# Kernel optimization log

Hardware: AMD Instinct MI355X
Metric: run time of the kernel (lower is better)

Reference implementation:

```python
import jax, jax.numpy as jnp
import numpy as np

B, N = 16, 128
DN0, DE0, DH = 64, 16, 128  # input node dim, input edge dim, hidden dim


def _gnn2(A, x, e, w_msg, b_msg, w_node, b_node):
    """One GNN2 layer on dense batched graphs.
    A: [B,N,N] adjacency mask, x: [B,N,Dn], e: [B,N,N,De].
    Message/new-edge: relu(Linear([x_i, x_j, e_ij])) masked by A.
    New node: relu(Linear([x, sum_j msg_ij])).
    The concat-Linear is decomposed into three matmuls to avoid
    materializing the [B,N,N,2Dn+De] concat tensor.
    """
    Dn = x.shape[-1]
    Wi, Wj, We = w_msg[:Dn], w_msg[Dn:2 * Dn], w_msg[2 * Dn:]
    xi = x @ Wi                                   # [B,N,Do]
    xj = x @ Wj                                   # [B,N,Do]
    msg = jax.nn.relu(xi[:, :, None, :] + xj[:, None, :, :] + e @ We + b_msg)
    msg = msg * A[..., None]                      # mask non-edges -> new edge_attr [B,N,N,Do]
    agg = msg.sum(axis=2)                         # scatter-sum over neighbors j -> [B,N,Do]
    Wx, Wa = w_node[:Dn], w_node[Dn:]
    x_new = jax.nn.relu(x @ Wx + agg @ Wa + b_node)
    return x_new, msg


def setup_inputs() -> dict:
    key = jax.random.key(0)
    ks = iter(jax.random.split(key, 32))
    s = 0.05
    inp = {
        "edge_index": jax.random.randint(next(ks), (B, N, N), 0, 2, dtype=jnp.int32),
        "x": jax.random.normal(next(ks), (B, N, DN0), dtype=jnp.float32),
        "edge_attr": jax.random.normal(next(ks), (B, N, N, DE0), dtype=jnp.float32),
    }
    def w(shape):
        return s * jax.random.normal(next(ks), shape, dtype=jnp.float32)
    # layer 0: node_in=64, edge_in=16 -> 128
    inp["w_msg_0"], inp["b_msg_0"] = w((2 * DN0 + DE0, DH)), w((DH,))
    inp["w_node_0"], inp["b_node_0"] = w((DN0 + DH, DH)), w((DH,))
    # layers 1,2: 128 -> 128
    for l in (1, 2):
        inp[f"w_msg_{l}"], inp[f"b_msg_{l}"] = w((2 * DH + DH, DH)), w((DH,))
        inp[f"w_node_{l}"], inp[f"b_node_{l}"] = w((DH + DH, DH)), w((DH,))
    # head mlp: 128 -> 128 -> 128 -> 1
    inp["w_h1"], inp["b_h1"] = w((DH, DH)), w((DH,))
    inp["w_h2"], inp["b_h2"] = w((DH, DH)), w((DH,))
    inp["w_h3"], inp["b_h3"] = w((DH, 1)), w((1,))
    return inp


def reference(edge_index, x, edge_attr,
              w_msg_0, b_msg_0, w_node_0, b_node_0,
              w_msg_1, b_msg_1, w_node_1, b_node_1,
              w_msg_2, b_msg_2, w_node_2, b_node_2,
              w_h1, b_h1, w_h2, b_h2, w_h3, b_h3):
    A = edge_index.astype(jnp.float32)
    x = x.astype(jnp.float32)
    # layer 0
    x, e = _gnn2(A, x, edge_attr, w_msg_0, b_msg_0, w_node_0, b_node_0)
    # middle layer with 0.5 residual blend
    x_, e_ = _gnn2(A, x, e, w_msg_1, b_msg_1, w_node_1, b_node_1)
    x = 0.5 * (x + x_)
    e = 0.5 * (e + e_)
    # last layer
    x, e = _gnn2(A, x, e, w_msg_2, b_msg_2, w_node_2, b_node_2)
    # edge_mean readout + MLP head
    h = e.mean(axis=(1, 2))                       # [B, DH]
    h = jax.nn.relu(h @ w_h1 + b_h1)
    h = jax.nn.relu(h @ w_h2 + b_h2)
    out = h @ w_h3 + b_h3                         # [B, 1]
    return out.squeeze(-1)                        # [B]
```

## Files before the change

kernel.cpp:

```cpp
#include <hip/hip_runtime.h>

constexpr int B = 16, N = 128, D = 128, DN0 = 64, DE0 = 16;

typedef _Float16 half8 __attribute__((ext_vector_type(8)));
typedef _Float16 half4 __attribute__((ext_vector_type(4)));
typedef float floatx4 __attribute__((ext_vector_type(4)));
typedef float floatx16 __attribute__((ext_vector_type(16)));

__device__ __forceinline__ void gld16(const _Float16* g, _Float16* l) {
  __builtin_amdgcn_global_load_lds(
      (const __attribute__((address_space(1))) void*)g,
      (__attribute__((address_space(3))) void*)l, 16, 0, 0);
}

__global__ __launch_bounds__(256) void k_pre(
    const float* __restrict__ x, const float* __restrict__ wm0,
    const float* __restrict__ bm0, const float* __restrict__ wm1,
    const float* __restrict__ wm2,
    float* __restrict__ xi0, float* __restrict__ xj0,
    _Float16* __restrict__ weT1, _Float16* __restrict__ weT2) {
  const int bid = blockIdx.x;
  const int t = threadIdx.x;
  if (bid < 512) {
    const int r0 = bid * 4;
    const int half = t >> 7, c = t & 127;
    __shared__ float sX[4][DN0];
    ((float*)sX)[t] = x[(size_t)r0 * DN0 + t];
    __syncthreads();
    float acc[4];
    #pragma unroll
    for (int r = 0; r < 4; ++r) acc[r] = half ? 0.f : bm0[c];
    const float* wb0 = wm0 + half * DN0 * D;
    #pragma unroll 4
    for (int k4 = 0; k4 < DN0; k4 += 4) {
      const float* wb = wb0 + k4 * D + c;
      const float w0 = wb[0], w1 = wb[D], w2 = wb[2 * D], w3 = wb[3 * D];
      #pragma unroll
      for (int r = 0; r < 4; ++r) {
        const float4 xv = *(const float4*)&sX[r][k4];
        acc[r] = fmaf(xv.x, w0, acc[r]);
        acc[r] = fmaf(xv.y, w1, acc[r]);
        acc[r] = fmaf(xv.z, w2, acc[r]);
        acc[r] = fmaf(xv.w, w3, acc[r]);
      }
    }
    float* dst = half ? xj0 : xi0;
    #pragma unroll
    for (int r = 0; r < 4; ++r) dst[(size_t)(r0 + r) * D + c] = acc[r];
  } else {
    const int g = (bid - 512) * 256 + t;
    const int layer = g >> 14;
    const int rem = g & 16383;
    const int c = rem >> 7, k = rem & 127;
    const float* src = layer ? wm2 : wm1;
    _Float16* dst = layer ? weT2 : weT1;
    dst[rem] = (_Float16)src[(2 * D + k) * D + c];
  }
}

__global__ __launch_bounds__(256) void k_edge0(
    const int* __restrict__ ei, const float* __restrict__ eattr,
    const float* __restrict__ wm0,
    const float* __restrict__ xi0, const float* __restrict__ xj0,
    _Float16* __restrict__ msg0, float* __restrict__ agg0) {
  const int row = blockIdx.x;
  const int b = row >> 7;
  const int t = threadIdx.x;
  const int c8 = (t & 15) * 8, jr = t >> 4;

  __shared__ float eb[N * 20];
  __shared__ float w_t[DE0][D];
  __shared__ float amask[N];
  __shared__ float xi_r[D];
  float* hp = eb;

  const float4* esrc = (const float4*)(eattr + (size_t)row * N * DE0);
  const float4* wsrc = (const float4*)(wm0 + 2 * DN0 * D);
  #pragma unroll
  for (int u = 0; u < 2; ++u) {
    const int idx4 = u * 256 + t;
    const int j = idx4 >> 2;
    const int k4 = (idx4 & 3) * 4;
    *(float4*)&eb[j * 20 + k4] = esrc[idx4];
    ((float4*)&w_t[0][0])[idx4] = wsrc[idx4];
  }
  if (t < N) {
    amask[t] = (float)ei[(size_t)row * N + t];
    xi_r[t] = xi0[(size_t)row * D + t];
  }
  __syncthreads();

  float acc[8][8] = {};
  #pragma unroll 4
  for (int k = 0; k < DE0; ++k) {
    float av[8];
    #pragma unroll
    for (int p = 0; p < 8; ++p) av[p] = eb[(16 * p + jr) * 20 + k];
    const floatx4 wv0 = *(const floatx4*)&w_t[k][c8];
    const floatx4 wv1 = *(const floatx4*)&w_t[k][c8 + 4];
    #pragma unroll
    for (int p = 0; p < 8; ++p)
      #pragma unroll
      for (int q = 0; q < 4; ++q) {
        acc[p][q]     = fmaf(av[p], wv0[q], acc[p][q]);
        acc[p][4 + q] = fmaf(av[p], wv1[q], acc[p][4 + q]);
      }
  }

  float acc8[8] = {};
  const float* xjb = xj0 + (size_t)b * N * D;
  _Float16* mrow = msg0 + (size_t)row * N * D;
  const floatx4 xiv0 = *(const floatx4*)&xi_r[c8];
  const floatx4 xiv1 = *(const floatx4*)&xi_r[c8 + 4];
  #pragma unroll
  for (int p = 0; p < 8; ++p) {
    const int j = 16 * p + jr;
    const float am = amask[j];
    const floatx4 xjv0 = *(const floatx4*)&xjb[j * D + c8];
    const floatx4 xjv1 = *(const floatx4*)&xjb[j * D + c8 + 4];
    half8 hv;
    #pragma unroll
    for (int q = 0; q < 4; ++q) {
      float v0 = fmaxf(xiv0[q] + xjv0[q] + acc[p][q], 0.f) * am;
      float v1 = fmaxf(xiv1[q] + xjv1[q] + acc[p][4 + q], 0.f) * am;
      hv[q] = (_Float16)v0;
      hv[4 + q] = (_Float16)v1;
      acc8[q] += v0;
      acc8[4 + q] += v1;
    }
    *(half8*)&mrow[j * D + (((t & 15) ^ jr) << 3)] = hv;
  }

  __syncthreads();
  #pragma unroll
  for (int q = 0; q < 8; ++q) hp[(jr * 16 + (t & 15)) * 8 + q] = acc8[q];
  __syncthreads();
  if (t < D) {
    float s = 0.f;
    #pragma unroll
    for (int g = 0; g < 16; ++g) s += hp[(g * 16 + (t >> 3)) * 8 + (t & 7)];
    agg0[(size_t)row * D + t] = s;
  }
}

__global__ __launch_bounds__(256) void k_node1(
    const float* __restrict__ x0, const float* __restrict__ agg0,
    const float* __restrict__ wn0, const float* __restrict__ bn0,
    const float* __restrict__ wm1, const float* __restrict__ bm1,
    float* __restrict__ x1, float* __restrict__ xi1, float* __restrict__ xj1) {
  const int r0 = blockIdx.x * 4;
  const int t = threadIdx.x;
  const int c = t & 127, rh = t >> 7;
  __shared__ float sIn[4][DN0];
  __shared__ float sAg[4][D];
  __shared__ float sX1[4][D];
  ((float*)sIn)[t] = x0[(size_t)r0 * DN0 + t];
  ((float2*)sAg)[t] = ((const float2*)(agg0 + (size_t)r0 * D))[t];
  __syncthreads();

  float acc[2];
  #pragma unroll
  for (int r = 0; r < 2; ++r) acc[r] = bn0[c];
  #pragma unroll 4
  for (int k4 = 0; k4 < DN0; k4 += 4) {
    const float* wb = wn0 + k4 * D + c;
    const float w0 = wb[0], w1 = wb[D], w2 = wb[2 * D], w3 = wb[3 * D];
    #pragma unroll
    for (int r = 0; r < 2; ++r) {
      const float4 xv = *(const float4*)&sIn[rh * 2 + r][k4];
      acc[r] = fmaf(xv.x, w0, acc[r]);
      acc[r] = fmaf(xv.y, w1, acc[r]);
      acc[r] = fmaf(xv.z, w2, acc[r]);
      acc[r] = fmaf(xv.w, w3, acc[r]);
    }
  }
  #pragma unroll 4
  for (int k4 = 0; k4 < D; k4 += 4) {
    const float* wb = wn0 + (DN0 + k4) * D + c;
    const float w0 = wb[0], w1 = wb[D], w2 = wb[2 * D], w3 = wb[3 * D];
    #pragma unroll
    for (int r = 0; r < 2; ++r) {
      const float4 xv = *(const float4*)&sAg[rh * 2 + r][k4];
      acc[r] = fmaf(xv.x, w0, acc[r]);
      acc[r] = fmaf(xv.y, w1, acc[r]);
      acc[r] = fmaf(xv.z, w2, acc[r]);
      acc[r] = fmaf(xv.w, w3, acc[r]);
    }
  }
  #pragma unroll
  for (int r = 0; r < 2; ++r) {
    const float v = fmaxf(acc[r], 0.f);
    sX1[rh * 2 + r][c] = v;
    x1[(size_t)(r0 + rh * 2 + r) * D + c] = v;
  }
  __syncthreads();

  float a[4];
  #pragma unroll
  for (int r = 0; r < 4; ++r) a[r] = rh ? 0.f : bm1[c];
  const float* wh = wm1 + (size_t)rh * D * D;
  #pragma unroll 4
  for (int k4 = 0; k4 < D; k4 += 4) {
    const float* wb = wh + k4 * D + c;
    const float w0 = wb[0], w1 = wb[D], w2 = wb[2 * D], w3 = wb[3 * D];
    #pragma unroll
    for (int r = 0; r < 4; ++r) {
      const float4 xv = *(const float4*)&sX1[r][k4];
      a[r] = fmaf(xv.x, w0, a[r]);
      a[r] = fmaf(xv.y, w1, a[r]);
      a[r] = fmaf(xv.z, w2, a[r]);
      a[r] = fmaf(xv.w, w3, a[r]);
    }
  }
  float* dst = rh ? xj1 : xi1;
  #pragma unroll
  for (int r = 0; r < 4; ++r) dst[(size_t)(r0 + r) * D + c] = a[r];
}

__global__ __launch_bounds__(256, 2) void k_mid(
    const int* __restrict__ ei, const _Float16* __restrict__ weT1,
    const _Float16* __restrict__ weT2,
    const float* __restrict__ xi, const float* __restrict__ xj,
    _Float16* __restrict__ em,
    float* __restrict__ agg1) {
  const int row = blockIdx.x;
  const int b = row >> 7;
  const int t = threadIdx.x;
  const int w = t >> 6;
  const int lane = t & 63;
  const int l31 = lane & 31;
  const int l15 = lane & 15;
  const int hl = lane >> 5;

  __shared__ _Float16 sE[N * D];
  __shared__ float sMask[N];

  const _Float16* gsrc = em + (size_t)row * N * D;
  #pragma unroll
  for (int u = 0; u < 8; ++u) {
    const int seg = (u * 4 + w) * 512;
    gld16(gsrc + seg + lane * 8, &sE[seg]);
  }

  half8 a1[8];
  #pragma unroll
  for (int ks = 0; ks < 8; ++ks)
    a1[ks] = *(const half8*)(weT1 + (32 * w + l31) * D + 16 * ks + 8 * hl);

  floatx4 xiv[4];
  #pragma unroll
  for (int g = 0; g < 4; ++g)
    xiv[g] = *(const floatx4*)&xi[(size_t)row * D + 32 * w + 8 * g + 4 * hl];
  if (t < N) sMask[t] = (float)ei[(size_t)row * N + t];

  __syncthreads();

  float am[4];
  #pragma unroll
  for (int jt = 0; jt < 4; ++jt) am[jt] = sMask[32 * jt + l31];

  const floatx16 vzero = {0.f,0.f,0.f,0.f,0.f,0.f,0.f,0.f,
                          0.f,0.f,0.f,0.f,0.f,0.f,0.f,0.f};
  floatx16 acc[4];
  #pragma unroll
  for (int jt = 0; jt < 4; ++jt) acc[jt] = vzero;
  #pragma unroll
  for (int ks = 0; ks < 8; ++ks)
    #pragma unroll
    for (int jt = 0; jt < 4; ++jt) {
      const half8 bv = *(const half8*)
          &sE[(32 * jt + l31) * D + (((2 * ks + hl) ^ l15) << 3)];
      acc[jt] = __builtin_amdgcn_mfma_f32_32x32x16_f16(a1[ks], bv, acc[jt], 0, 0, 0);
    }

  __syncthreads();

  const float* xjb = xj + (size_t)b * N * D;
  floatx4 hacc[4];
  #pragma unroll
  for (int g = 0; g < 4; ++g) hacc[g] = (floatx4){0.f, 0.f, 0.f, 0.f};
  #pragma unroll
  for (int jt = 0; jt < 4; ++jt) {
    const int j = 32 * jt + l31;
    #pragma unroll
    for (int g = 0; g < 4; ++g) {
      const int cofs = 32 * w + 8 * g + 4 * hl;
      const int hidx = j * D + (((4 * w + g) ^ l15) << 3) + 4 * hl;
      const floatx4 xjv = *(const floatx4*)&xjb[j * D + cofs];
      const half4 m0 = *(const half4*)&sE[hidx];
      half4 mid;
      floatx4 m1;
      #pragma unroll
      for (int r = 0; r < 4; ++r) {
        const float v = xiv[g][r] + xjv[r] + acc[jt][4 * g + r];
        m1[r] = fmaxf(v, 0.f) * am[jt];
        mid[r] = (_Float16)(0.5f * ((float)m0[r] + m1[r]));
      }
      *(half4*)&sE[hidx] = mid;
      hacc[g] += m1;
    }
  }

  #pragma unroll
  for (int m = 1; m < 32; m <<= 1)
    #pragma unroll
    for (int g = 0; g < 4; ++g)
      #pragma unroll
      for (int r = 0; r < 4; ++r)
        hacc[g][r] += __shfl_xor(hacc[g][r], m, 64);
  if (l31 == 0) {
    #pragma unroll
    for (int g = 0; g < 4; ++g)
      *(floatx4*)&agg1[(size_t)row * D + 32 * w + 8 * g + 4 * hl] = hacc[g];
  }

  half8 a2[8];
  #pragma unroll
  for (int ks = 0; ks < 8; ++ks)
    a2[ks] = *(const half8*)(weT2 + (32 * w + l31) * D + 16 * ks + 8 * hl);

  __syncthreads();

  #pragma unroll
  for (int jt = 0; jt < 4; ++jt) acc[jt] = vzero;
  #pragma unroll
  for (int ks = 0; ks < 8; ++ks)
    #pragma unroll
    for (int jt = 0; jt < 4; ++jt) {
      const half8 bv = *(const half8*)
          &sE[(32 * jt + l31) * D + (((2 * ks + hl) ^ l15) << 3)];
      acc[jt] = __builtin_amdgcn_mfma_f32_32x32x16_f16(a2[ks], bv, acc[jt], 0, 0, 0);
    }

  __syncthreads();

  #pragma unroll
  for (int jt = 0; jt < 4; ++jt) {
    const int j = 32 * jt + l31;
    #pragma unroll
    for (int g = 0; g < 4; ++g) {
      const int hidx = j * D + (((4 * w + g) ^ l15) << 3) + 4 * hl;
      half4 tv;
      #pragma unroll
      for (int r = 0; r < 4; ++r) tv[r] = (_Float16)acc[jt][4 * g + r];
      *(half4*)&sE[hidx] = tv;
    }
  }

  __syncthreads();

  uint4* gdst = (uint4*)(em + (size_t)row * N * D);
  const uint4* ls = (const uint4*)sE;
  #pragma unroll
  for (int u = 0; u < 8; ++u) {
    const int idx4 = u * 256 + t;
    const int j = u * 16 + (t >> 4);
    if (sMask[j] != 0.f) gdst[idx4] = ls[idx4];
  }
}

__global__ __launch_bounds__(256) void k_node2(
    const float* __restrict__ x1, const float* __restrict__ agg1,
    const float* __restrict__ wn1, const float* __restrict__ bn1,
    const float* __restrict__ wm2, const float* __restrict__ bm2,
    float* __restrict__ xi2, float* __restrict__ xj2) {
  const int r0 = blockIdx.x * 4;
  const int t = threadIdx.x;
  const int c = t & 127, rh = t >> 7;
  __shared__ float sIn[4][D];
  __shared__ float sAg[4][D];
  __shared__ float sXm[4][D];
  ((float2*)sIn)[t] = ((const float2*)(x1 + (size_t)r0 * D))[t];
  ((float2*)sAg)[t] = ((const float2*)(agg1 + (size_t)r0 * D))[t];
  __syncthreads();

  float acc[2];
  #pragma unroll
  for (int r = 0; r < 2; ++r) acc[r] = bn1[c];
  #pragma unroll 4
  for (int k4 = 0; k4 < D; k4 += 4) {
    const float* wb = wn1 + k4 * D + c;
    const float w0 = wb[0], w1 = wb[D], w2 = wb[2 * D], w3 = wb[3 * D];
    #pragma unroll
    for (int r = 0; r < 2; ++r) {
      const float4 xv = *(const float4*)&sIn[rh * 2 + r][k4];
      acc[r] = fmaf(xv.x, w0, acc[r]);
      acc[r] = fmaf(xv.y, w1, acc[r]);
      acc[r] = fmaf(xv.z, w2, acc[r]);
      acc[r] = fmaf(xv.w, w3, acc[r]);
    }
  }
  #pragma unroll 4
  for (int k4 = 0; k4 < D; k4 += 4) {
    const float* wb = wn1 + (D + k4) * D + c;
    const float w0 = wb[0], w1 = wb[D], w2 = wb[2 * D], w3 = wb[3 * D];
    #pragma unroll
    for (int r = 0; r < 2; ++r) {
      const float4 xv = *(const float4*)&sAg[rh * 2 + r][k4];
      acc[r] = fmaf(xv.x, w0, acc[r]);
      acc[r] = fmaf(xv.y, w1, acc[r]);
      acc[r] = fmaf(xv.z, w2, acc[r]);
      acc[r] = fmaf(xv.w, w3, acc[r]);
    }
  }
  #pragma unroll
  for (int r = 0; r < 2; ++r) {
    const float v = 0.5f * (sIn[rh * 2 + r][c] + fmaxf(acc[r], 0.f));
    sXm[rh * 2 + r][c] = v;
  }
  __syncthreads();

  float a[4];
  #pragma unroll
  for (int r = 0; r < 4; ++r) a[r] = rh ? 0.f : bm2[c];
  const float* wh = wm2 + (size_t)rh * D * D;
  #pragma unroll 4
  for (int k4 = 0; k4 < D; k4 += 4) {
    const float* wb = wh + k4 * D + c;
    const float w0 = wb[0], w1 = wb[D], w2 = wb[2 * D], w3 = wb[3 * D];
    #pragma unroll
    for (int r = 0; r < 4; ++r) {
      const float4 xv = *(const float4*)&sXm[r][k4];
      a[r] = fmaf(xv.x, w0, a[r]);
      a[r] = fmaf(xv.y, w1, a[r]);
      a[r] = fmaf(xv.z, w2, a[r]);
      a[r] = fmaf(xv.w, w3, a[r]);
    }
  }
  float* dst = rh ? xj2 : xi2;
  #pragma unroll
  for (int r = 0; r < 4; ++r) dst[(size_t)(r0 + r) * D + c] = a[r];
}

__global__ __launch_bounds__(256) void k_fin(
    const int* __restrict__ ei, const _Float16* __restrict__ t2,
    const float* __restrict__ xi, const float* __restrict__ xj,
    float* __restrict__ rowsum) {
  const int row = blockIdx.x;
  const int b = row >> 7;
  const int t = threadIdx.x;
  const int c8 = (t & 15) * 8, jr = t >> 4;

  __shared__ float sMask[N];
  __shared__ float hp[16][16][8];
  if (t < N) sMask[t] = (float)ei[(size_t)row * N + t];
  float xiv[8];
  *(floatx4*)&xiv[0] = *(const floatx4*)&xi[row * D + c8];
  *(floatx4*)&xiv[4] = *(const floatx4*)&xi[row * D + c8 + 4];
  __syncthreads();

  const _Float16* src = t2 + (size_t)row * N * D;
  const float* xjb = xj + (size_t)b * N * D;
  float acc8[8] = {};
  #pragma unroll
  for (int u = 0; u < 8; ++u) {
    const int j = u * 16 + jr;
    if (sMask[j] != 0.f) {
      const half8 tv = *(const half8*)(src + j * D + (((t & 15) ^ jr) << 3));
      const floatx4 xj0 = *(const floatx4*)&xjb[j * D + c8];
      const floatx4 xj1 = *(const floatx4*)&xjb[j * D + c8 + 4];
      #pragma unroll
      for (int r = 0; r < 4; ++r) {
        acc8[r]     += fmaxf(xiv[r] + xj0[r] + (float)tv[r], 0.f);
        acc8[4 + r] += fmaxf(xiv[4 + r] + xj1[r] + (float)tv[4 + r], 0.f);
      }
    }
  }
  #pragma unroll
  for (int k = 0; k < 8; ++k) hp[jr][t & 15][k] = acc8[k];
  __syncthreads();
  if (t < D) {
    float s = 0.f;
    #pragma unroll
    for (int g = 0; g < 16; ++g) s += hp[g][t >> 3][t & 7];
    rowsum[row * D + t] = s;
  }
}

__global__ __launch_bounds__(128) void k_head(
    const float* __restrict__ rowsum,
    const float* __restrict__ w1, const float* __restrict__ b1,
    const float* __restrict__ w2, const float* __restrict__ b2,
    const float* __restrict__ w3, const float* __restrict__ b3,
    float* __restrict__ out) {
  const int b = blockIdx.x;
  const int c = threadIdx.x;
  __shared__ float hr[D], h1r[D], h2r[D];
  const float* rs = rowsum + (size_t)b * N * D;
  float s = 0.f;
  for (int i = 0; i < N; ++i) s += rs[i * D + c];
  hr[c] = s * (1.f / (N * N));
  __syncthreads();
  float a = b1[c];
  #pragma unroll 8
  for (int k = 0; k < D; ++k) a = fmaf(hr[k], w1[k * D + c], a);
  h1r[c] = fmaxf(a, 0.f);
  __syncthreads();
  a = b2[c];
  #pragma unroll 8
  for (int k = 0; k < D; ++k) a = fmaf(h1r[k], w2[k * D + c], a);
  h2r[c] = fmaxf(a, 0.f);
  __syncthreads();
  hr[c] = h2r[c] * w3[c];
  __syncthreads();
  if (c == 0) {
    float s2 = b3[0];
    for (int k = 0; k < D; ++k) s2 += hr[k];
    out[b] = s2;
  }
}

extern "C" void kernel_launch(void* const* d_in, const int* in_sizes, int n_in,
                              void* d_out, int out_size, void* d_ws, size_t ws_size,
                              hipStream_t stream) {
  const int*   ei  = (const int*)d_in[0];
  const float* x0  = (const float*)d_in[1];
  const float* ea  = (const float*)d_in[2];
  const float* wm0 = (const float*)d_in[3];
  const float* bm0 = (const float*)d_in[4];
  const float* wn0 = (const float*)d_in[5];
  const float* bn0 = (const float*)d_in[6];
  const float* wm1 = (const float*)d_in[7];
  const float* bm1 = (const float*)d_in[8];
  const float* wn1 = (const float*)d_in[9];
  const float* bn1 = (const float*)d_in[10];
  const float* wm2 = (const float*)d_in[11];
  const float* bm2 = (const float*)d_in[12];
  const float* wh1 = (const float*)d_in[15];
  const float* bh1 = (const float*)d_in[16];
  const float* wh2 = (const float*)d_in[17];
  const float* bh2 = (const float*)d_in[18];
  const float* wh3 = (const float*)d_in[19];
  const float* bh3 = (const float*)d_in[20];
  float* out = (float*)d_out;

  _Float16* msg0h = (_Float16*)d_ws;
  _Float16* weT1  = msg0h + (size_t)B * N * N * D;
  _Float16* weT2  = weT1 + D * D;
  float* f = (float*)(weT2 + D * D);
  size_t off = 0;
  const size_t R = (size_t)B * N * D;
  float* xi0  = f + off; off += R;
  float* xj0  = f + off; off += R;
  float* x1   = f + off; off += R;
  float* xi1  = f + off; off += R;
  float* xj1  = f + off; off += R;
  float* xi2  = f + off; off += R;
  float* xj2  = f + off; off += R;
  float* rsum = f + off; off += R;

  float* aggS = rsum;

  const int rows = B * N;
  k_pre  <<<512 + 128, 256, 0, stream>>>(x0, wm0, bm0, wm1, wm2,
                                         xi0, xj0, weT1, weT2);
  k_edge0<<<rows, 256, 0, stream>>>(ei, ea, wm0, xi0, xj0, msg0h, aggS);
  k_node1<<<rows / 4, 256, 0, stream>>>(x0, aggS, wn0, bn0, wm1, bm1,
                                        x1, xi1, xj1);
  k_mid  <<<rows, 256, 0, stream>>>(ei, weT1, weT2, xi1, xj1, msg0h, aggS);
  k_node2<<<rows / 4, 256, 0, stream>>>(x1, aggS, wn1, bn1, wm2, bm2,
                                        xi2, xj2);
  k_fin  <<<rows, 256, 0, stream>>>(ei, msg0h, xi2, xj2, rsum);
  k_head <<<B,    128, 0, stream>>>(rsum, wh1, bh1, wh2, bh2, wh3, bh3, out);
}
```

Measured before the change: 214.0 us.

## Give each wave its own 32 edge rows in k_mid to drop block barriers

k_mid now splits the work so each wave owns 32 neighbor rows j and computes all 128 output columns for them, rather than owning 32 output columns across all rows. Each wave touches only its own slice of shared memory, so almost every __syncthreads between the two MFMA stages is removed. The edge tile is loaded per wave with an explicit vmcnt wait, and the mask comes from a register plus shuffles instead of shared memory. The cost is that weight fragments are re-read from global or L2 inside the MFMA loop instead of staying in registers, and per-wave partial aggregates must be combined through shared memory at the end.

```diff
diff --git a/kernel.cpp b/kernel.cpp
--- a/kernel.cpp
+++ b/kernel.cpp
@@ -231,132 +231,121 @@
   const int l31 = lane & 31;
   const int l15 = lane & 15;
   const int hl = lane >> 5;
+  const int j = 32 * w + l31;
 
   __shared__ _Float16 sE[N * D];
-  __shared__ float sMask[N];
+  __shared__ float sAggP[4][D];
 
   const _Float16* gsrc = em + (size_t)row * N * D;
   #pragma unroll
   for (int u = 0; u < 8; ++u) {
-    const int seg = (u * 4 + w) * 512;
+    const int seg = w * 4096 + u * 512;
     gld16(gsrc + seg + lane * 8, &sE[seg]);
   }
 
-  half8 a1[8];
+  const float am = (float)ei[(size_t)row * N + j];
+
+  asm volatile("s_waitcnt vmcnt(0)" ::: "memory");
+  __builtin_amdgcn_sched_barrier(0);
+
+  half8 bv[8];
   #pragma unroll
   for (int ks = 0; ks < 8; ++ks)
-    a1[ks] = *(const half8*)(weT1 + (32 * w + l31) * D + 16 * ks + 8 * hl);
-
-  floatx4 xiv[4];
-  #pragma unroll
-  for (int g = 0; g < 4; ++g)
-    xiv[g] = *(const floatx4*)&xi[(size_t)row * D + 32 * w + 8 * g + 4 * hl];
-  if (t < N) sMask[t] = (float)ei[(size_t)row * N + t];
-
-  __syncthreads();
-
-  float am[4];
-  #pragma unroll
-  for (int jt = 0; jt < 4; ++jt) am[jt] = sMask[32 * jt + l31];
+    bv[ks] = *(const half8*)&sE[j * D + (((2 * ks + hl) ^ l15) << 3)];
 
   const floatx16 vzero = {0.f,0.f,0.f,0.f,0.f,0.f,0.f,0.f,
                           0.f,0.f,0.f,0.f,0.f,0.f,0.f,0.f};
   floatx16 acc[4];
   #pragma unroll
-  for (int jt = 0; jt < 4; ++jt) acc[jt] = vzero;
-  #pragma unroll
-  for (int ks = 0; ks < 8; ++ks)
-    #pragma unroll
-    for (int jt = 0; jt < 4; ++jt) {
-      const half8 bv = *(const half8*)
-          &sE[(32 * jt + l31) * D + (((2 * ks + hl) ^ l15) << 3)];
-      acc[jt] = __builtin_amdgcn_mfma_f32_32x32x16_f16(a1[ks], bv, acc[jt], 0, 0, 0);
-    }
-
-  __syncthreads();
+  for (int ct = 0; ct < 4; ++ct) acc[ct] = vzero;
+  #pragma unroll
+  for (int ct = 0; ct < 4; ++ct)
+    #pragma unroll
+    for (int ks = 0; ks < 8; ++ks) {
+      const half8 av = *(const half8*)
+          &weT1[(32 * ct + l31) * D + 16 * ks + 8 * hl];
+      acc[ct] = __builtin_amdgcn_mfma_f32_32x32x16_f16(av, bv[ks], acc[ct], 0, 0, 0);
+    }
 
   const float* xjb = xj + (size_t)b * N * D;
-  floatx4 hacc[4];
-  #pragma unroll
-  for (int g = 0; g < 4; ++g) hacc[g] = (floatx4){0.f, 0.f, 0.f, 0.f};
-  #pragma unroll
-  for (int jt = 0; jt < 4; ++jt) {
-    const int j = 32 * jt + l31;
+  const float* xir = xi + (size_t)row * D;
+  #pragma unroll
+  for (int ct = 0; ct < 4; ++ct) {
+    floatx4 hacc[4];
+    #pragma unroll
+    for (int g = 0; g < 4; ++g) hacc[g] = (floatx4){0.f, 0.f, 0.f, 0.f};
     #pragma unroll
     for (int g = 0; g < 4; ++g) {
-      const int cofs = 32 * w + 8 * g + 4 * hl;
-      const int hidx = j * D + (((4 * w + g) ^ l15) << 3) + 4 * hl;
-      const floatx4 xjv = *(const floatx4*)&xjb[j * D + cofs];
+      const int co = 32 * ct + 8 * g + 4 * hl;
+      const int hidx = j * D + (((4 * ct + g) ^ l15) << 3) + 4 * hl;
+      const floatx4 xiv = *(const floatx4*)&xir[co];
+      const floatx4 xjv = *(const floatx4*)&xjb[j * D + co];
       const half4 m0 = *(const half4*)&sE[hidx];
       half4 mid;
       floatx4 m1;
       #pragma unroll
       for (int r = 0; r < 4; ++r) {
-        const float v = xiv[g][r] + xjv[r] + acc[jt][4 * g + r];
-        m1[r] = fmaxf(v, 0.f) * am[jt];
+        const float v = xiv[r] + xjv[r] + acc[ct][4 * g + r];
+        m1[r] = fmaxf(v, 0.f) * am;
         mid[r] = (_Float16)(0.5f * ((float)m0[r] + m1[r]));
       }
       *(half4*)&sE[hidx] = mid;
       hacc[g] += m1;
     }
-  }
-
-  #pragma unroll
-  for (int m = 1; m < 32; m <<= 1)
-    #pragma unroll
-    for (int g = 0; g < 4; ++g)
-      #pragma unroll
-      for (int r = 0; r < 4; ++r)
-        hacc[g][r] += __shfl_xor(hacc[g][r], m, 64);
-  if (l31 == 0) {
-    #pragma unroll
-    for (int g = 0; g < 4; ++g)
-      *(floatx4*)&agg1[(size_t)row * D + 32 * w + 8 * g + 4 * hl] = hacc[g];
-  }
-
-  half8 a2[8];
+    #pragma unroll
+    for (int m = 1; m < 32; m <<= 1)
+      #pragma unroll
+      for (int g = 0; g < 4; ++g)
+        #pragma unroll
+        for (int r = 0; r < 4; ++r)
+          hacc[g][r] += __shfl_xor(hacc[g][r], m, 64);
+    if (l31 == 0) {
+      #pragma unroll
+      for (int g = 0; g < 4; ++g)
+        *(floatx4*)&sAggP[w][32 * ct + 8 * g + 4 * hl] = hacc[g];
+    }
+  }
+
+  half8 bv2[8];
   #pragma unroll
   for (int ks = 0; ks < 8; ++ks)
-    a2[ks] = *(const half8*)(weT2 + (32 * w + l31) * D + 16 * ks + 8 * hl);
-
-  __syncthreads();
-
-  #pragma unroll
-  for (int jt = 0; jt < 4; ++jt) acc[jt] = vzero;
-  #pragma unroll
-  for (int ks = 0; ks < 8; ++ks)
-    #pragma unroll
-    for (int jt = 0; jt < 4; ++jt) {
-      const half8 bv = *(const half8*)
-          &sE[(32 * jt + l31) * D + (((2 * ks + hl) ^ l15) << 3)];
-      acc[jt] = __builtin_amdgcn_mfma_f32_32x32x16_f16(a2[ks], bv, acc[jt], 0, 0, 0);
-    }
-
-  __syncthreads();
-
-  #pragma unroll
-  for (int jt = 0; jt < 4; ++jt) {
-    const int j = 32 * jt + l31;
+    bv2[ks] = *(const half8*)&sE[j * D + (((2 * ks + hl) ^ l15) << 3)];
+  #pragma unroll
+  for (int ct = 0; ct < 4; ++ct) acc[ct] = vzero;
+  #pragma unroll
+  for (int ct = 0; ct < 4; ++ct)
+    #pragma unroll
+    for (int ks = 0; ks < 8; ++ks) {
+      const half8 av = *(const half8*)
+          &weT2[(32 * ct + l31) * D + 16 * ks + 8 * hl];
+      acc[ct] = __builtin_amdgcn_mfma_f32_32x32x16_f16(av, bv2[ks], acc[ct], 0, 0, 0);
+    }
+
+  #pragma unroll
+  for (int ct = 0; ct < 4; ++ct)
     #pragma unroll
     for (int g = 0; g < 4; ++g) {
-      const int hidx = j * D + (((4 * w + g) ^ l15) << 3) + 4 * hl;
+      const int hidx = j * D + (((4 * ct + g) ^ l15) << 3) + 4 * hl;
       half4 tv;
       #pragma unroll
-      for (int r = 0; r < 4; ++r) tv[r] = (_Float16)acc[jt][4 * g + r];
+      for (int r = 0; r < 4; ++r) tv[r] = (_Float16)acc[ct][4 * g + r];
       *(half4*)&sE[hidx] = tv;
     }
-  }
-
-  __syncthreads();
 
   uint4* gdst = (uint4*)(em + (size_t)row * N * D);
   const uint4* ls = (const uint4*)sE;
   #pragma unroll
   for (int u = 0; u < 8; ++u) {
-    const int idx4 = u * 256 + t;
-    const int j = u * 16 + (t >> 4);
-    if (sMask[j] != 0.f) gdst[idx4] = ls[idx4];
-  }
+    const int cc = u * 64 + lane;
+    const int idx4 = w * 512 + cc;
+    const float mv = __shfl(am, cc >> 4, 64);
+    if (mv != 0.f) gdst[idx4] = ls[idx4];
+  }
+
+  __syncthreads();
+  if (t < D)
+    agg1[(size_t)row * D + t] =
+        sAggP[0][t] + sAggP[1][t] + sAggP[2][t] + sAggP[3][t];
 }
 
 __global__ __launch_bounds__(256) void k_node2(
```

After: 257.0 us. 1.2x slower.

## Recompute layer-0 edge messages inside k_mid instead of storing them

Applied to the files above, without the earlier changes.

k_edge0 now only computes the aggregated sums and no longer writes the fp16 layer-0 message tensor. k_mid recomputes the layer-0 messages directly into shared memory from edge_attr, the edge weight slice and xi0/xj0. This removes a full B*N*N*D fp16 write and the matching read, which is a large memory round trip. The cost is doing the small K=16 edge matmul twice, plus extra shared memory and register pressure in k_mid, which may reduce its occupancy.

```diff
diff --git a/kernel.cpp b/kernel.cpp
--- a/kernel.cpp
+++ b/kernel.cpp
@@ -6,12 +6,6 @@
 typedef _Float16 half4 __attribute__((ext_vector_type(4)));
 typedef float floatx4 __attribute__((ext_vector_type(4)));
 typedef float floatx16 __attribute__((ext_vector_type(16)));
-
-__device__ __forceinline__ void gld16(const _Float16* g, _Float16* l) {
-  __builtin_amdgcn_global_load_lds(
-      (const __attribute__((address_space(1))) void*)g,
-      (__attribute__((address_space(3))) void*)l, 16, 0, 0);
-}
 
 __global__ __launch_bounds__(256) void k_pre(
     const float* __restrict__ x, const float* __restrict__ wm0,
@@ -62,7 +56,7 @@
     const int* __restrict__ ei, const float* __restrict__ eattr,
     const float* __restrict__ wm0,
     const float* __restrict__ xi0, const float* __restrict__ xj0,
-    _Float16* __restrict__ msg0, float* __restrict__ agg0) {
+    float* __restrict__ agg0) {
   const int row = blockIdx.x;
   const int b = row >> 7;
   const int t = threadIdx.x;
@@ -109,7 +103,6 @@
 
   float acc8[8] = {};
   const float* xjb = xj0 + (size_t)b * N * D;
-  _Float16* mrow = msg0 + (size_t)row * N * D;
   const floatx4 xiv0 = *(const floatx4*)&xi_r[c8];
   const floatx4 xiv1 = *(const floatx4*)&xi_r[c8 + 4];
   #pragma unroll
@@ -118,17 +111,11 @@
     const float am = amask[j];
     const floatx4 xjv0 = *(const floatx4*)&xjb[j * D + c8];
     const floatx4 xjv1 = *(const floatx4*)&xjb[j * D + c8 + 4];
-    half8 hv;
     #pragma unroll
     for (int q = 0; q < 4; ++q) {
-      float v0 = fmaxf(xiv0[q] + xjv0[q] + acc[p][q], 0.f) * am;
-      float v1 = fmaxf(xiv1[q] + xjv1[q] + acc[p][4 + q], 0.f) * am;
-      hv[q] = (_Float16)v0;
-      hv[4 + q] = (_Float16)v1;
-      acc8[q] += v0;
-      acc8[4 + q] += v1;
-    }
-    *(half8*)&mrow[j * D + (((t & 15) ^ jr) << 3)] = hv;
+      acc8[q]     += fmaxf(xiv0[q] + xjv0[q] + acc[p][q], 0.f) * am;
+      acc8[4 + q] += fmaxf(xiv1[q] + xjv1[q] + acc[p][4 + q], 0.f) * am;
+    }
   }
 
   __syncthreads();
@@ -218,8 +205,10 @@
 }
 
 __global__ __launch_bounds__(256, 2) void k_mid(
-    const int* __restrict__ ei, const _Float16* __restrict__ weT1,
-    const _Float16* __restrict__ weT2,
+    const int* __restrict__ ei, const float* __restrict__ eattr,
+    const float* __restrict__ wm0,
+    const float* __restrict__ xi0, const float* __restrict__ xj0,
+    const _Float16* __restrict__ weT1, const _Float16* __restrict__ weT2,
     const float* __restrict__ xi, const float* __restrict__ xj,
     _Float16* __restrict__ em,
     float* __restrict__ agg1) {
@@ -233,14 +222,65 @@
   const int hl = lane >> 5;
 
   __shared__ _Float16 sE[N * D];
-  __shared__ float sMask[N];
-
-  const _Float16* gsrc = em + (size_t)row * N * D;
-  #pragma unroll
-  for (int u = 0; u < 8; ++u) {
-    const int seg = (u * 4 + w) * 512;
-    gld16(gsrc + seg + lane * 8, &sE[seg]);
-  }
+  __shared__ float eb[N * 20];
+  __shared__ float w_t[DE0][D];
+  __shared__ float amask[N];
+  __shared__ float xi0r[D];
+
+  {
+    const int c8 = (t & 15) * 8, jr = t >> 4;
+    const float4* esrc = (const float4*)(eattr + (size_t)row * N * DE0);
+    const float4* wsrc = (const float4*)(wm0 + 2 * DN0 * D);
+    #pragma unroll
+    for (int u = 0; u < 2; ++u) {
+      const int idx4 = u * 256 + t;
+      const int j = idx4 >> 2;
+      const int k4 = (idx4 & 3) * 4;
+      *(float4*)&eb[j * 20 + k4] = esrc[idx4];
+      ((float4*)&w_t[0][0])[idx4] = wsrc[idx4];
+    }
+    if (t < N) {
+      amask[t] = (float)ei[(size_t)row * N + t];
+      xi0r[t] = xi0[(size_t)row * D + t];
+    }
+    __syncthreads();
+
+    float acc[8][8] = {};
+    #pragma unroll 4
+    for (int k = 0; k < DE0; ++k) {
+      float av[8];
+      #pragma unroll
+      for (int p = 0; p < 8; ++p) av[p] = eb[(16 * p + jr) * 20 + k];
+      const floatx4 wv0 = *(const floatx4*)&w_t[k][c8];
+      const floatx4 wv1 = *(const floatx4*)&w_t[k][c8 + 4];
+      #pragma unroll
+      for (int p = 0; p < 8; ++p)
+        #pragma unroll
+        for (int q = 0; q < 4; ++q) {
+          acc[p][q]     = fmaf(av[p], wv0[q], acc[p][q]);
+          acc[p][4 + q] = fmaf(av[p], wv1[q], acc[p][4 + q]);
+        }
+    }
+
+    const float* xjb0 = xj0 + (size_t)b * N * D;
+    const floatx4 xiv0 = *(const floatx4*)&xi0r[c8];
+    const floatx4 xiv1 = *(const floatx4*)&xi0r[c8 + 4];
+    #pragma unroll
+    for (int p = 0; p < 8; ++p) {
+      const int j = 16 * p + jr;
+      const float am = amask[j];
+      const floatx4 xjv0 = *(const floatx4*)&xjb0[j * D + c8];
+      const floatx4 xjv1 = *(const floatx4*)&xjb0[j * D + c8 + 4];
+      half8 hv;
+      #pragma unroll
+      for (int q = 0; q < 4; ++q) {
+        hv[q]     = (_Float16)(fmaxf(xiv0[q] + xjv0[q] + acc[p][q], 0.f) * am);
+        hv[4 + q] = (_Float16)(fmaxf(xiv1[q] + xjv1[q] + acc[p][4 + q], 0.f) * am);
+      }
+      *(half8*)&sE[j * D + (((t & 15) ^ jr) << 3)] = hv;
+    }
+  }
+  __syncthreads();
 
   half8 a1[8];
   #pragma unroll
@@ -251,13 +291,10 @@
   #pragma unroll
   for (int g = 0; g < 4; ++g)
     xiv[g] = *(const floatx4*)&xi[(size_t)row * D + 32 * w + 8 * g + 4 * hl];
-  if (t < N) sMask[t] = (float)ei[(size_t)row * N + t];
-
-  __syncthreads();
 
   float am[4];
   #pragma unroll
-  for (int jt = 0; jt < 4; ++jt) am[jt] = sMask[32 * jt + l31];
+  for (int jt = 0; jt < 4; ++jt) am[jt] = amask[32 * jt + l31];
 
   const floatx16 vzero = {0.f,0.f,0.f,0.f,0.f,0.f,0.f,0.f,
                           0.f,0.f,0.f,0.f,0.f,0.f,0.f,0.f};
@@ -355,7 +392,7 @@
   for (int u = 0; u < 8; ++u) {
     const int idx4 = u * 256 + t;
     const int j = u * 16 + (t >> 4);
-    if (sMask[j] != 0.f) gdst[idx4] = ls[idx4];
+    if (amask[j] != 0.f) gdst[idx4] = ls[idx4];
   }
 }
 
@@ -554,10 +591,11 @@
   const int rows = B * N;
   k_pre  <<<512 + 128, 256, 0, stream>>>(x0, wm0, bm0, wm1, wm2,
                                          xi0, xj0, weT1, weT2);
-  k_edge0<<<rows, 256, 0, stream>>>(ei, ea, wm0, xi0, xj0, msg0h, aggS);
+  k_edge0<<<rows, 256, 0, stream>>>(ei, ea, wm0, xi0, xj0, aggS);
   k_node1<<<rows / 4, 256, 0, stream>>>(x0, aggS, wn0, bn0, wm1, bm1,
                                         x1, xi1, xj1);
-  k_mid  <<<rows, 256, 0, stream>>>(ei, weT1, weT2, xi1, xj1, msg0h, aggS);
+  k_mid  <<<rows, 256, 0, stream>>>(ei, ea, wm0, xi0, xj0, weT1, weT2,
+                                    xi1, xj1, msg0h, aggS);
   k_node2<<<rows / 4, 256, 0, stream>>>(x1, aggS, wn1, bn1, wm2, bm2,
                                         xi2, xj2);
   k_fin  <<<rows, 256, 0, stream>>>(ei, msg0h, xi2, xj2, rsum);
```

New measurement: 217.7 us. About the same (+1.7%).

## Process two node rows per block in k_mid to reuse weight fragments

Applied to the files above, without the earlier changes.

k_mid now handles two consecutive rows i per block, staging both edge tiles in LDS (64 KB) and issuing interleaved MFMAs with shared A fragments for both. This amortizes weight-fragment register loads and per-block overhead, and puts two independent MFMA chains in flight. In exchange LDS use doubles, so only one or two blocks fit per CU, the grid halves to 1024 blocks, and doubled accumulator registers may raise pressure or cause spills.

```diff
diff --git a/kernel.cpp b/kernel.cpp
--- a/kernel.cpp
+++ b/kernel.cpp
@@ -223,8 +223,8 @@
     const float* __restrict__ xi, const float* __restrict__ xj,
     _Float16* __restrict__ em,
     float* __restrict__ agg1) {
-  const int row = blockIdx.x;
-  const int b = row >> 7;
+  const int row0 = blockIdx.x * 2;
+  const int b = row0 >> 7;
   const int t = threadIdx.x;
   const int w = t >> 6;
   const int lane = t & 63;
@@ -232,14 +232,21 @@
   const int l15 = lane & 15;
   const int hl = lane >> 5;
 
-  __shared__ _Float16 sE[N * D];
-  __shared__ float sMask[N];
-
-  const _Float16* gsrc = em + (size_t)row * N * D;
+  __shared__ _Float16 sE0[N * D];
+  __shared__ _Float16 sE1[N * D];
+  __shared__ float sMask[2][N];
+
+  const _Float16* gsrc0 = em + (size_t)row0 * N * D;
+  const _Float16* gsrc1 = em + (size_t)(row0 + 1) * N * D;
   #pragma unroll
   for (int u = 0; u < 8; ++u) {
     const int seg = (u * 4 + w) * 512;
-    gld16(gsrc + seg + lane * 8, &sE[seg]);
+    gld16(gsrc0 + seg + lane * 8, &sE0[seg]);
+  }
+  #pragma unroll
+  for (int u = 0; u < 8; ++u) {
+    const int seg = (u * 4 + w) * 512;
+    gld16(gsrc1 + seg + lane * 8, &sE1[seg]);
   }
 
   half8 a1[8];
@@ -247,115 +254,172 @@
   for (int ks = 0; ks < 8; ++ks)
     a1[ks] = *(const half8*)(weT1 + (32 * w + l31) * D + 16 * ks + 8 * hl);
 
-  floatx4 xiv[4];
-  #pragma unroll
-  for (int g = 0; g < 4; ++g)
-    xiv[g] = *(const floatx4*)&xi[(size_t)row * D + 32 * w + 8 * g + 4 * hl];
-  if (t < N) sMask[t] = (float)ei[(size_t)row * N + t];
-
-  __syncthreads();
-
-  float am[4];
-  #pragma unroll
-  for (int jt = 0; jt < 4; ++jt) am[jt] = sMask[32 * jt + l31];
+  floatx4 xiv0[4], xiv1[4];
+  #pragma unroll
+  for (int g = 0; g < 4; ++g) {
+    xiv0[g] = *(const floatx4*)&xi[(size_t)row0 * D + 32 * w + 8 * g + 4 * hl];
+    xiv1[g] = *(const floatx4*)
+        &xi[(size_t)(row0 + 1) * D + 32 * w + 8 * g + 4 * hl];
+  }
+  sMask[t >> 7][t & 127] = (float)ei[(size_t)(row0 + (t >> 7)) * N + (t & 127)];
+
+  __syncthreads();
+
+  float am0[4], am1[4];
+  #pragma unroll
+  for (int jt = 0; jt < 4; ++jt) {
+    am0[jt] = sMask[0][32 * jt + l31];
+    am1[jt] = sMask[1][32 * jt + l31];
+  }
 
   const floatx16 vzero = {0.f,0.f,0.f,0.f,0.f,0.f,0.f,0.f,
                           0.f,0.f,0.f,0.f,0.f,0.f,0.f,0.f};
-  floatx16 acc[4];
-  #pragma unroll
-  for (int jt = 0; jt < 4; ++jt) acc[jt] = vzero;
+  floatx16 accA[4], accB[4];
+  #pragma unroll
+  for (int jt = 0; jt < 4; ++jt) { accA[jt] = vzero; accB[jt] = vzero; }
   #pragma unroll
   for (int ks = 0; ks < 8; ++ks)
     #pragma unroll
     for (int jt = 0; jt < 4; ++jt) {
-      const half8 bv = *(const half8*)
-          &sE[(32 * jt + l31) * D + (((2 * ks + hl) ^ l15) << 3)];
-      acc[jt] = __builtin_amdgcn_mfma_f32_32x32x16_f16(a1[ks], bv, acc[jt], 0, 0, 0);
+      const int bofs = (32 * jt + l31) * D + (((2 * ks + hl) ^ l15) << 3);
+      const half8 bv0 = *(const half8*)&sE0[bofs];
+      accA[jt] = __builtin_amdgcn_mfma_f32_32x32x16_f16(a1[ks], bv0, accA[jt], 0, 0, 0);
+      const half8 bv1 = *(const half8*)&sE1[bofs];
+      accB[jt] = __builtin_amdgcn_mfma_f32_32x32x16_f16(a1[ks], bv1, accB[jt], 0, 0, 0);
     }
 
   __syncthreads();
 
   const float* xjb = xj + (size_t)b * N * D;
-  floatx4 hacc[4];
-  #pragma unroll
-  for (int g = 0; g < 4; ++g) hacc[g] = (floatx4){0.f, 0.f, 0.f, 0.f};
+  {
+    floatx4 hacc[4];
+    #pragma unroll
+    for (int g = 0; g < 4; ++g) hacc[g] = (floatx4){0.f, 0.f, 0.f, 0.f};
+    #pragma unroll
+    for (int jt = 0; jt < 4; ++jt) {
+      const int j = 32 * jt + l31;
+      #pragma unroll
+      for (int g = 0; g < 4; ++g) {
+        const int cofs = 32 * w + 8 * g + 4 * hl;
+        const int hidx = j * D + (((4 * w + g) ^ l15) << 3) + 4 * hl;
+        const floatx4 xjv = *(const floatx4*)&xjb[j * D + cofs];
+        const half4 m0 = *(const half4*)&sE0[hidx];
+        half4 mid;
+        floatx4 m1;
+        #pragma unroll
+        for (int r = 0; r < 4; ++r) {
+          const float v = xiv0[g][r] + xjv[r] + accA[jt][4 * g + r];
+          m1[r] = fmaxf(v, 0.f) * am0[jt];
+          mid[r] = (_Float16)(0.5f * ((float)m0[r] + m1[r]));
+        }
+        *(half4*)&sE0[hidx] = mid;
+        hacc[g] += m1;
+      }
+    }
+    #pragma unroll
+    for (int m = 1; m < 32; m <<= 1)
+      #pragma unroll
+      for (int g = 0; g < 4; ++g)
+        #pragma unroll
+        for (int r = 0; r < 4; ++r)
+          hacc[g][r] += __shfl_xor(hacc[g][r], m, 64);
+    if (l31 == 0) {
+      #pragma unroll
+      for (int g = 0; g < 4; ++g)
+        *(floatx4*)&agg1[(size_t)row0 * D + 32 * w + 8 * g + 4 * hl] = hacc[g];
+    }
+  }
+  {
+    floatx4 hacc[4];
+    #pragma unroll
+    for (int g = 0; g < 4; ++g) hacc[g] = (floatx4){0.f, 0.f, 0.f, 0.f};
+    #pragma unroll
+    for (int jt = 0; jt < 4; ++jt) {
+      const int j = 32 * jt + l31;
+      #pragma unroll
+      for (int g = 0; g < 4; ++g) {
+        const int cofs = 32 * w + 8 * g + 4 * hl;
+        const int hidx = j * D + (((4 * w + g) ^ l15) << 3) + 4 * hl;
+        const floatx4 xjv = *(const floatx4*)&xjb[j * D + cofs];
+        const half4 m0 = *(const half4*)&sE1[hidx];
+        half4 mid;
+        floatx4 m1;
+        #pragma unroll
+        for (int r = 0; r < 4; ++r) {
+          const float v = xiv1[g][r] + xjv[r] + accB[jt][4 * g + r];
+          m1[r] = fmaxf(v, 0.f) * am1[jt];
+          mid[r] = (_Float16)(0.5f * ((float)m0[r] + m1[r]));
+        }
+        *(half4*)&sE1[hidx] = mid;
+        hacc[g] += m1;
+      }
+    }
+    #pragma unroll
+    for (int m = 1; m < 32; m <<= 1)
+      #pragma unroll
+      for (int g = 0; g < 4; ++g)
+        #pragma unroll
+        for (int r = 0; r < 4; ++r)
+          hacc[g][r] += __shfl_xor(hacc[g][r], m, 64);
+    if (l31 == 0) {
+      #pragma unroll
+      for (int g = 0; g < 4; ++g)
+        *(floatx4*)&agg1[(size_t)(row0 + 1) * D + 32 * w + 8 * g + 4 * hl] =
+            hacc[g];
+    }
+  }
+
+  half8 a2[8];
+  #pragma unroll
+  for (int ks = 0; ks < 8; ++ks)
+    a2[ks] = *(const half8*)(weT2 + (32 * w + l31) * D + 16 * ks + 8 * hl);
+
+  __syncthreads();
+
+  #pragma unroll
+  for (int jt = 0; jt < 4; ++jt) { accA[jt] = vzero; accB[jt] = vzero; }
+  #pragma unroll
+  for (int ks = 0; ks < 8; ++ks)
+    #pragma unroll
+    for (int jt = 0; jt < 4; ++jt) {
+      const int bofs = (32 * jt + l31) * D + (((2 * ks + hl) ^ l15) << 3);
+      const half8 bv0 = *(const half8*)&sE0[bofs];
+      accA[jt] = __builtin_amdgcn_mfma_f32_32x32x16_f16(a2[ks], bv0, accA[jt], 0, 0, 0);
+      const half8 bv1 = *(const half8*)&sE1[bofs];
+      accB[jt] = __builtin_amdgcn_mfma_f32_32x32x16_f16(a2[ks], bv1, accB[jt], 0, 0, 0);
+    }
+
+  __syncthreads();
+
   #pragma unroll
   for (int jt = 0; jt < 4; ++jt) {
     const int j = 32 * jt + l31;
     #pragma unroll
     for (int g = 0; g < 4; ++g) {
-      const int cofs = 32 * w + 8 * g + 4 * hl;
       const int hidx = j * D + (((4 * w + g) ^ l15) << 3) + 4 * hl;
-      const floatx4 xjv = *(const floatx4*)&xjb[j * D + cofs];
-      const half4 m0 = *(const half4*)&sE[hidx];
-      half4 mid;
-      floatx4 m1;
+      half4 tv0, tv1;
       #pragma unroll
       for (int r = 0; r < 4; ++r) {
-        const float v = xiv[g][r] + xjv[r] + acc[jt][4 * g + r];
-        m1[r] = fmaxf(v, 0.f) * am[jt];
-        mid[r] = (_Float16)(0.5f * ((float)m0[r] + m1[r]));
+        tv0[r] = (_Float16)accA[jt][4 * g + r];
+        tv1[r] = (_Float16)accB[jt][4 * g + r];
       }
-      *(half4*)&sE[hidx] = mid;
-      hacc[g] += m1;
-    }
-  }
-
-  #pragma unroll
-  for (int m = 1; m < 32; m <<= 1)
-    #pragma unroll
-    for (int g = 0; g < 4; ++g)
-      #pragma unroll
-      for (int r = 0; r < 4; ++r)
-        hacc[g][r] += __shfl_xor(hacc[g][r], m, 64);
-  if (l31 == 0) {
-    #pragma unroll
-    for (int g = 0; g < 4; ++g)
-      *(floatx4*)&agg1[(size_t)row * D + 32 * w + 8 * g + 4 * hl] = hacc[g];
-  }
-
-  half8 a2[8];
-  #pragma unroll
-  for (int ks = 0; ks < 8; ++ks)
-    a2[ks] = *(const half8*)(weT2 + (32 * w + l31) * D + 16 * ks + 8 * hl);
-
-  __syncthreads();
-
-  #pragma unroll
-  for (int jt = 0; jt < 4; ++jt) acc[jt] = vzero;
-  #pragma unroll
-  for (int ks = 0; ks < 8; ++ks)
-    #pragma unroll
-    for (int jt = 0; jt < 4; ++jt) {
-      const half8 bv = *(const half8*)
-          &sE[(32 * jt + l31) * D + (((2 * ks + hl) ^ l15) << 3)];
-      acc[jt] = __builtin_amdgcn_mfma_f32_32x32x16_f16(a2[ks], bv, acc[jt], 0, 0, 0);
-    }
-
-  __syncthreads();
-
-  #pragma unroll
-  for (int jt = 0; jt < 4; ++jt) {
-    const int j = 32 * jt + l31;
-    #pragma unroll
-    for (int g = 0; g < 4; ++g) {
-      const int hidx = j * D + (((4 * w + g) ^ l15) << 3) + 4 * hl;
-      half4 tv;
-      #pragma unroll
-      for (int r = 0; r < 4; ++r) tv[r] = (_Float16)acc[jt][4 * g + r];
-      *(half4*)&sE[hidx] = tv;
-    }
-  }
-
-  __syncthreads();
-
-  uint4* gdst = (uint4*)(em + (size_t)row * N * D);
-  const uint4* ls = (const uint4*)sE;
+      *(half4*)&sE0[hidx] = tv0;
+      *(half4*)&sE1[hidx] = tv1;
+    }
+  }
+
+  __syncthreads();
+
+  uint4* gdst0 = (uint4*)(em + (size_t)row0 * N * D);
+  uint4* gdst1 = (uint4*)(em + (size_t)(row0 + 1) * N * D);
+  const uint4* ls0 = (const uint4*)sE0;
+  const uint4* ls1 = (const uint4*)sE1;
   #pragma unroll
   for (int u = 0; u < 8; ++u) {
     const int idx4 = u * 256 + t;
     const int j = u * 16 + (t >> 4);
-    if (sMask[j] != 0.f) gdst[idx4] = ls[idx4];
+    if (sMask[0][j] != 0.f) gdst0[idx4] = ls0[idx4];
+    if (sMask[1][j] != 0.f) gdst1[idx4] = ls1[idx4];
   }
 }
 
@@ -557,7 +621,8 @@
   k_edge0<<<rows, 256, 0, stream>>>(ei, ea, wm0, xi0, xj0, msg0h, aggS);
   k_node1<<<rows / 4, 256, 0, stream>>>(x0, aggS, wn0, bn0, wm1, bm1,
                                         x1, xi1, xj1);
-  k_mid  <<<rows, 256, 0, stream>>>(ei, weT1, weT2, xi1, xj1, msg0h, aggS);
+  k_mid  <<<rows / 2, 256, 0, stream>>>(ei, weT1, weT2, xi1, xj1, msg0h,
+                                        aggS);
   k_node2<<<rows / 4, 256, 0, stream>>>(x1, aggS, wn1, bn1, wm2, bm2,
                                         xi2, xj2);
   k_fin  <<<rows, 256, 0, stream>>>(ei, msg0h, xi2, xj2, rsum);
```

Result: no change. 211.7 us, median of 2 (-1.1%).
